# Kernel tuning notes

Measured on AMD Instinct MI355X. Metric: run time of the kernel, lower is better.

## Reference

```python
import jax, jax.numpy as jnp
import numpy as np

B, T, C, H = 8, 1024, 768, 12
HD = C // H  # head_dim = 64


def setup_inputs() -> dict:
    key = jax.random.key(0)
    ks = jax.random.split(key, 5)
    x = jax.random.normal(ks[0], (B, T, C), dtype=jnp.float32)
    mask = jnp.tril(jnp.ones((T, T), dtype=bool))[None, None, :, :]  # causal [1,1,T,T]
    # Dense params (flax Dense: y = x @ kernel + bias)
    W_qkv = jax.random.normal(ks[1], (C, 3 * C), dtype=jnp.float32) * (1.0 / np.sqrt(C))
    b_qkv = jnp.zeros((3 * C,), dtype=jnp.float32)
    W_proj = jax.random.normal(ks[2], (C, C), dtype=jnp.float32) * (1.0 / np.sqrt(C))
    b_proj = jnp.zeros((C,), dtype=jnp.float32)
    return {"x": x, "mask": mask, "W_qkv": W_qkv, "b_qkv": b_qkv,
            "W_proj": W_proj, "b_proj": b_proj}


def reference(x, mask, W_qkv, b_qkv, W_proj, b_proj):
    Bx, Tx, Cx = x.shape
    qkv = x @ W_qkv + b_qkv                      # [B, T, 3C]
    qkv = qkv.reshape(Bx, Tx, 3 * H, HD)
    q, k, v = jnp.array_split(qkv, 3, axis=2)    # each [B, T, H, HD]
    scale = 1.0 / jnp.sqrt(jnp.float32(HD))
    attn = jnp.einsum('bqhd,bkhd->bhqk', q, k) * scale  # [B, H, T, T]
    attn = jnp.where(mask, attn, jnp.finfo(jnp.float32).min)
    attn = jax.nn.softmax(attn, axis=-1)
    out = jnp.einsum('bhqk,bkhd->bqhd', attn, v).reshape(Bx, Tx, Cx)
    return out @ W_proj + b_proj
```

## Files before the change

kernel.cpp:

```cpp
#include <hip/hip_runtime.h>


typedef unsigned short u16;
typedef unsigned int u32;
typedef __bf16 bf16x8 __attribute__((ext_vector_type(8)));
typedef float  f32x4  __attribute__((ext_vector_type(4)));
typedef float  f32x16 __attribute__((ext_vector_type(16)));
typedef unsigned short u16x4 __attribute__((ext_vector_type(4)));
typedef unsigned short u16x8 __attribute__((ext_vector_type(8)));
typedef unsigned int u32x4 __attribute__((ext_vector_type(4)));

#define DEV static __device__ __forceinline__

constexpr int B_ = 8, T_ = 1024, C_ = 768, H_ = 12, HD_ = 64;
constexpr int M1 = B_ * T_;
constexpr int N1 = 3 * C_;
constexpr int KD = C_;

DEV u16 f2bf(float f) {
    union { float f; unsigned u; } v; v.f = f;
    unsigned r = v.u + 0x7fffu + ((v.u >> 16) & 1u);
    return (u16)(r >> 16);
}

DEV u16 bfbits(float f) {
    __bf16 h = (__bf16)f;
    union { __bf16 h; u16 u; } v; v.h = h;
    return v.u;
}

DEV u32 cvtpk(float lo, float hi) {
    u32 r;
    asm("v_cvt_pk_bf16_f32 %0, %1, %2" : "=v"(r) : "v"(lo), "v"(hi));
    return r;
}

DEV void gload16(const void* g, void* l) {
    __builtin_amdgcn_global_load_lds(
        (const __attribute__((address_space(1))) unsigned*)g,
        (__attribute__((address_space(3))) unsigned*)l, 16, 0, 0);
}

DEV float redmax16(f32x16 v) {
    float a0 = fmaxf(v[0], v[1]), a1 = fmaxf(v[2], v[3]);
    float a2 = fmaxf(v[4], v[5]), a3 = fmaxf(v[6], v[7]);
    float a4 = fmaxf(v[8], v[9]), a5 = fmaxf(v[10], v[11]);
    float a6 = fmaxf(v[12], v[13]), a7 = fmaxf(v[14], v[15]);
    float b0 = fmaxf(a0, a1), b1 = fmaxf(a2, a3);
    float b2 = fmaxf(a4, a5), b3 = fmaxf(a6, a7);
    return fmaxf(fmaxf(b0, b1), fmaxf(b2, b3));
}
DEV float redsum16(f32x16 v) {
    float a0 = v[0] + v[1], a1 = v[2] + v[3], a2 = v[4] + v[5], a3 = v[6] + v[7];
    float a4 = v[8] + v[9], a5 = v[10] + v[11], a6 = v[12] + v[13], a7 = v[14] + v[15];
    float b0 = a0 + a1, b1 = a2 + a3, b2 = a4 + a5, b3 = a6 + a7;
    return (b0 + b1) + (b2 + b3);
}


__global__ __launch_bounds__(256) void cvt_all_kern(
    const float* __restrict__ x, u16* __restrict__ xb,
    const float* __restrict__ Wq, const float* __restrict__ Wp,
    u16* __restrict__ WqT, u16* __restrict__ WpT) {
    __shared__ float tile[32][33];
    const int bid = blockIdx.x;
    if (bid < 3072) {
        const int i = bid * 256 + threadIdx.x;
        const float4* xf = (const float4*)x;
        float4 a = xf[i * 2], b = xf[i * 2 + 1];
        u16x8 o;
        o[0] = f2bf(a.x); o[1] = f2bf(a.y); o[2] = f2bf(a.z); o[3] = f2bf(a.w);
        o[4] = f2bf(b.x); o[5] = f2bf(b.y); o[6] = f2bf(b.z); o[7] = f2bf(b.w);
        *(u16x8*)(xb + (size_t)i * 8) = o;
        return;
    }
    const int wb = bid - 3072;
    int bx = wb % 96;
    const int k0 = (wb / 96) * 32;
    const float* W; u16* Wt; int N;
    if (bx < N1 / 32) { W = Wq; Wt = WqT; N = N1; }
    else { bx -= N1 / 32; W = Wp; Wt = WpT; N = C_; }
    const int n0 = bx * 32;
    const int tx = threadIdx.x & 31, ty = threadIdx.x >> 5;
#pragma unroll
    for (int i = 0; i < 4; i++) {
        int k = ty * 4 + i;
        tile[k][tx] = W[(size_t)(k0 + k) * N + n0 + tx];
    }
    __syncthreads();
#pragma unroll
    for (int i = 0; i < 4; i++) {
        int n = ty * 4 + i;
        Wt[(size_t)(n0 + n) * KD + k0 + tx] = f2bf(tile[tx][n]);
    }
}


template <int MODE>
__global__ __launch_bounds__(256, 2) void gemm_bt_kern(
    const u16* __restrict__ A, const u16* __restrict__ Bt,
    const float* __restrict__ bias, int nBN,
    u16* __restrict__ qw, u16* __restrict__ kw, u16* __restrict__ vw,
    float* __restrict__ out) {
    __shared__ u16 lds[16384];
    char* LA = (char*)lds;
    char* LB = (char*)lds + 16384;
    const int cpx = gridDim.x >> 3;
    const int bid = (blockIdx.x & 7) * cpx + (blockIdx.x >> 3);
    const int bm = bid / nBN, bn = bid % nBN;
    const int m0 = bm * 128, n0 = bn * 128;
    const int t = threadIdx.x;
    const int lane = t & 63, w = t >> 6;
    const int wr = w >> 1, wc = w & 1;
    const int l15 = lane & 15, lhi = lane >> 4;
    const int srow = t >> 3;
    const int scb = ((t & 7) << 4) ^ ((srow & 7) << 4);
    const char* Ab = (const char*)(A + (size_t)(m0 + srow) * KD) + scb;
    const char* Bb = (const char*)(Bt + (size_t)(n0 + srow) * KD) + scb;

    f32x4 acc[4][4] = {};

    for (int k0 = 0; k0 < KD; k0 += 64) {
#pragma unroll
        for (int s = 0; s < 4; s++) {
            gload16(Ab + (size_t)k0 * 2 + (size_t)s * 32 * KD * 2, LA + w * 1024 + s * 4096);
            gload16(Bb + (size_t)k0 * 2 + (size_t)s * 32 * KD * 2, LB + w * 1024 + s * 4096);
        }
        __syncthreads();
#pragma unroll
        for (int kk = 0; kk < 2; kk++) {
            bf16x8 af[4], bfr[4];
#pragma unroll
            for (int i = 0; i < 4; i++) {
                int rowA = wr * 64 + i * 16 + l15;
                af[i] = *(const bf16x8*)(LA + rowA * 128 +
                                         ((kk * 64 + lhi * 16) ^ ((rowA & 7) << 4)));
                int rowB = wc * 64 + i * 16 + l15;
                bfr[i] = *(const bf16x8*)(LB + rowB * 128 +
                                          ((kk * 64 + lhi * 16) ^ ((rowB & 7) << 4)));
            }
#pragma unroll
            for (int fm = 0; fm < 4; fm++)
#pragma unroll
                for (int fn = 0; fn < 4; fn++)
                    acc[fm][fn] = __builtin_amdgcn_mfma_f32_16x16x32_bf16(
                        af[fm], bfr[fn], acc[fm][fn], 0, 0, 0);
        }
        __syncthreads();
    }

    if constexpr (MODE == 1) {
#pragma unroll
        for (int fm = 0; fm < 4; fm++) {
            const int mb = m0 + wr * 64 + fm * 16 + lhi * 4;
#pragma unroll
            for (int fn = 0; fn < 4; fn++) {
                const int n = n0 + wc * 64 + fn * 16 + l15;
                const float bv = bias[n];
#pragma unroll
                for (int r = 0; r < 4; r++)
                    out[(size_t)(mb + r) * C_ + n] = acc[fm][fn][r] + bv;
            }
        }
    } else {
        char* TT = (char*)lds;
        const int typ = bn / 6;
        const int h0 = (bn % 6) * 2;
        if (typ < 2) {
            const float sc = (typ == 0) ? 0.125f * 1.44269504f : 1.0f;
#pragma unroll
            for (int fn = 0; fn < 4; fn++) {
                const int col = wc * 64 + fn * 16 + l15;
                const float bv = bias[n0 + col];
#pragma unroll
                for (int fm = 0; fm < 4; fm++) {
                    const int row0 = wr * 64 + fm * 16 + lhi * 4;
#pragma unroll
                    for (int r = 0; r < 4; r++) {
                        const int row = row0 + r;
                        *(u16*)(TT + row * 256 + ((col * 2) ^ ((row & 7) << 5))) =
                            bfbits((acc[fm][fn][r] + bv) * sc);
                    }
                }
            }
            __syncthreads();
            u16* dst = (typ == 0) ? qw : kw;
#pragma unroll
            for (int i = 0; i < 8; i++) {
                const int wk = t + 256 * i;
                const int m = wk >> 4, c = wk & 15;
                u16x8 v8 = *(u16x8*)(TT + m * 256 + ((c * 16) ^ ((m & 7) << 5)));
                const int mb = m0 + m, b = mb >> 10, tq = mb & 1023;
                const int h = h0 + (c >> 3), d0 = (c & 7) * 8;
                *(u16x8*)(dst + (((size_t)(b * H_ + h) * T_ + tq) << 6) + d0) = v8;
            }
        } else {
#pragma unroll
            for (int fn = 0; fn < 4; fn++) {
                const int col = wc * 64 + fn * 16 + l15;
                const float bv = bias[n0 + col];
                const int cx = (col & 7) << 4;
#pragma unroll
                for (int fm = 0; fm < 4; fm++) {
                    const int row0 = wr * 64 + fm * 16 + lhi * 4;
                    u16x4 pk;
#pragma unroll
                    for (int r = 0; r < 4; r++) pk[r] = bfbits(acc[fm][fn][r] + bv);
                    *(u16x4*)(TT + col * 256 + ((row0 * 2) ^ cx)) = pk;
                }
            }
            __syncthreads();
#pragma unroll
            for (int i = 0; i < 8; i++) {
                const int wk = t + 256 * i;
                const int col = wk >> 4, ch = wk & 15;
                u16x8 v8 = *(u16x8*)(TT + col * 256 + ((ch * 16) ^ ((col & 7) << 4)));
                const int b = m0 >> 10, tq0 = (m0 & 1023) + ch * 8;
                const int h = h0 + (col >> 6), d = col & 63;
                *(u16x8*)(vw + (((size_t)(b * H_ + h) * HD_ + d) << 10) + tq0) = v8;
            }
        }
    }
}


__global__ __launch_bounds__(256, 4) void attn_fwd_kern(
    const u16* __restrict__ qg, const u16* __restrict__ kg,
    const u16* __restrict__ vg, u16* __restrict__ ao) {
    __shared__ u16 kld[2][64 * 64];
    __shared__ u16 vld[2][64 * 64];
    const int n = blockIdx.x;
    const int bh = (n & 7) + 8 * ((n >> 3) % 12);
    const int qt = 7 - n / 96;
    const int t = threadIdx.x, lane = t & 63, w = t >> 6;
    const int q5 = lane & 31, h2 = lane >> 5;
    const int srow = t >> 3;
    const int scb = ((t & 7) << 4) ^ ((srow & 7) << 4);
    const char* kb = (const char*)(kg + (size_t)bh * T_ * HD_);
    const char* vb = (const char*)(vg + (size_t)bh * HD_ * T_);

    const int qrow_g = qt * 128 + w * 32 + q5;
    const u16* qrow = qg + (size_t)bh * T_ * HD_ + (size_t)qrow_g * HD_ + h2 * 8;
    bf16x8 qf[4];
#pragma unroll
    for (int kc = 0; kc < 4; kc++)
        qf[kc] = *(const bf16x8*)(qrow + kc * 16);

#pragma unroll
    for (int s = 0; s < 2; s++) {
        gload16(kb + (size_t)(srow + s * 32) * 128 + scb,
                (char*)kld[0] + w * 1024 + s * 4096);
        gload16(vb + (size_t)(srow + s * 32) * 2048 + scb,
                (char*)vld[0] + w * 1024 + s * 4096);
    }
    __syncthreads();

    f32x16 acc[2] = {};
    float mst = -1e30f, lst = 0.f;
    const int qmax = qt * 128 + w * 32 + 31;

    const int ntiles = 2 * qt + 2;
    for (int kvt = 0; kvt < ntiles; kvt++) {
        const int cur = kvt & 1;
        if (kvt + 1 < ntiles) {
#pragma unroll
            for (int s = 0; s < 2; s++) {
                gload16(kb + (size_t)((kvt + 1) * 64 + srow + s * 32) * 128 + scb,
                        (char*)kld[cur ^ 1] + w * 1024 + s * 4096);
                gload16(vb + (size_t)(srow + s * 32) * 2048 + (kvt + 1) * 128 + scb,
                        (char*)vld[cur ^ 1] + w * 1024 + s * 4096);
            }
        }
        if (kvt * 64 <= qmax) {
            const char* kbase = (const char*)kld[cur];
            const char* vbase = (const char*)vld[cur];
            f32x16 s0 = {}, s1 = {};
            __builtin_amdgcn_s_setprio(1);
#pragma unroll
            for (int kc = 0; kc < 4; kc++) {
                const int r0 = q5, r1 = 32 + q5;
                bf16x8 kf0 = *(const bf16x8*)(kbase + r0 * 128 +
                                              ((kc * 32 + h2 * 16) ^ ((r0 & 7) << 4)));
                bf16x8 kf1 = *(const bf16x8*)(kbase + r1 * 128 +
                                              ((kc * 32 + h2 * 16) ^ ((r1 & 7) << 4)));
                s0 = __builtin_amdgcn_mfma_f32_32x32x16_bf16(kf0, qf[kc], s0, 0, 0, 0);
                s1 = __builtin_amdgcn_mfma_f32_32x32x16_bf16(kf1, qf[kc], s1, 0, 0, 0);
            }
            __builtin_amdgcn_s_setprio(0);
            if (kvt * 64 + 63 > qt * 128 + w * 32) {
                const int qg_ = qrow_g, kvb0 = kvt * 64 + 4 * h2;
#pragma unroll
                for (int r = 0; r < 16; r++) {
                    const int kvo = (r & 3) + 8 * (r >> 2);
                    if (kvb0 + kvo > qg_) s0[r] = -1e30f;
                    if (kvb0 + 32 + kvo > qg_) s1[r] = -1e30f;
                }
            }
            float pmax = fmaxf(redmax16(s0), redmax16(s1));
            pmax = fmaxf(pmax, __shfl_xor(pmax, 32));
            if (!__all(pmax <= mst)) {
                const float mn = fmaxf(mst, pmax);
                const float corr = exp2f(mst - mn);
                mst = mn;
#pragma unroll
                for (int r = 0; r < 16; r++) { acc[0][r] *= corr; acc[1][r] *= corr; }
                lst *= corr;
            }
#pragma unroll
            for (int r = 0; r < 16; r++) {
                s0[r] = exp2f(s0[r] - mst);
                s1[r] = exp2f(s1[r] - mst);
            }
            float rs = redsum16(s0) + redsum16(s1);
            rs += __shfl_xor(rs, 32);
            lst += rs;
            u32 pw0[8], pw1[8];
#pragma unroll
            for (int i = 0; i < 4; i++) {
                pw0[i]     = cvtpk(s0[4 * i + 0], s0[4 * i + 1]);
                pw1[i]     = cvtpk(s0[4 * i + 2], s0[4 * i + 3]);
                pw0[i + 4] = cvtpk(s1[4 * i + 0], s1[4 * i + 1]);
                pw1[i + 4] = cvtpk(s1[4 * i + 2], s1[4 * i + 3]);
            }
            bf16x8 pf[4];
#pragma unroll
            for (int m = 0; m < 4; m++) {
                u32 a0 = pw0[2 * m], b0 = pw0[2 * m + 1];
                asm("v_permlane32_swap_b32 %0, %1" : "+v"(a0), "+v"(b0));
                u32 a1 = pw1[2 * m], b1 = pw1[2 * m + 1];
                asm("v_permlane32_swap_b32 %0, %1" : "+v"(a1), "+v"(b1));
                u32x4 wv; wv[0] = a0; wv[1] = a1; wv[2] = b0; wv[3] = b1;
                pf[m] = __builtin_bit_cast(bf16x8, wv);
            }
            __builtin_amdgcn_s_setprio(1);
#pragma unroll
            for (int m = 0; m < 4; m++) {
#pragma unroll
                for (int db = 0; db < 2; db++) {
                    const int rd = db * 32 + q5;
                    bf16x8 vf = *(const bf16x8*)(vbase + rd * 128 +
                                                 ((m * 32 + h2 * 16) ^ ((rd & 7) << 4)));
                    acc[db] = __builtin_amdgcn_mfma_f32_32x32x16_bf16(vf, pf[m], acc[db], 0, 0, 0);
                }
            }
            __builtin_amdgcn_s_setprio(0);
        }
        __syncthreads();
    }

    const int b = bh / H_, h = bh % H_;
    const float inv = 1.0f / lst;
    u16* orow = ao + (size_t)(b * T_ + qrow_g) * C_ + h * 64 + 4 * h2;
#pragma unroll
    for (int db = 0; db < 2; db++)
#pragma unroll
        for (int q2 = 0; q2 < 4; q2++) {
            u16x4 pk;
#pragma unroll
            for (int e = 0; e < 4; e++) pk[e] = bfbits(acc[db][q2 * 4 + e] * inv);
            *(u16x4*)(orow + db * 32 + q2 * 8) = pk;
        }
}


extern "C" void kernel_launch(void* const* d_in, const int* in_sizes, int n_in,
                              void* d_out, int out_size, void* d_ws, size_t ws_size,
                              hipStream_t stream) {
    const float* x     = (const float*)d_in[0];
    const float* Wqkv  = (const float*)d_in[2];
    const float* bqkv  = (const float*)d_in[3];
    const float* Wproj = (const float*)d_in[4];
    const float* bproj = (const float*)d_in[5];
    float* out = (float*)d_out;

    char* ws = (char*)d_ws;
    u16* xb     = (u16*)(ws);
    u16* wqkvT  = (u16*)(ws + 12582912);
    u16* wprojT = (u16*)(ws + 16121856);
    u16* qw     = (u16*)(ws + 17301504);
    u16* kw     = (u16*)(ws + 29884416);
    u16* vw     = (u16*)(ws + 42467328);
    u16* ao     = (u16*)(ws + 55050240);

    cvt_all_kern<<<5376, 256, 0, stream>>>(x, xb, Wqkv, Wproj, wqkvT, wprojT);

    gemm_bt_kern<0><<<(M1 / 128) * (N1 / 128), 256, 0, stream>>>(
        xb, wqkvT, bqkv, N1 / 128, qw, kw, vw, nullptr);

    attn_fwd_kern<<<B_ * H_ * (T_ / 128), 256, 0, stream>>>(qw, kw, vw, ao);

    gemm_bt_kern<1><<<(M1 / 128) * (C_ / 128), 256, 0, stream>>>(
        ao, wprojT, bproj, C_ / 128, nullptr, nullptr, nullptr, out);
}
```

Measured before the change: 102.9 us.

## Split attention KV range in two per query tile and merge partials

Each causal query tile's KV loop is split into two halves run by separate blocks, doubling the grid to improve load balance and occupancy across CUs. Each half writes a normalized bf16 partial output plus its running max and sum, and a new merge kernel combines them with softmax rescaling into the head-interleaved layout. This costs extra global traffic for partials, an extra kernel launch, and an additional bf16 rounding of partial outputs. The split path is enabled only when the workspace is large enough, and it reuses the xb buffer for one partial.

```diff
diff --git a/kernel.cpp b/kernel.cpp
--- a/kernel.cpp
+++ b/kernel.cpp
@@ -16,6 +16,7 @@
 constexpr int M1 = B_ * T_;
 constexpr int N1 = 3 * C_;
 constexpr int KD = C_;
+constexpr int NROW = B_ * H_ * T_;
 
 DEV u16 f2bf(float f) {
     union { float f; unsigned u; } v; v.f = f;
@@ -27,6 +28,11 @@
     __bf16 h = (__bf16)f;
     union { __bf16 h; u16 u; } v; v.h = h;
     return v.u;
+}
+
+DEV float bf2f(u16 x) {
+    union { u32 u; float f; } v; v.u = (u32)x << 16;
+    return v.f;
 }
 
 DEV u32 cvtpk(float lo, float hi) {
@@ -224,14 +230,26 @@
 }
 
 
+template <int SPLIT>
 __global__ __launch_bounds__(256, 4) void attn_fwd_kern(
     const u16* __restrict__ qg, const u16* __restrict__ kg,
-    const u16* __restrict__ vg, u16* __restrict__ ao) {
+    const u16* __restrict__ vg, u16* __restrict__ ao,
+    u16* __restrict__ On0, u16* __restrict__ On1, float* __restrict__ ml) {
     __shared__ u16 kld[2][64 * 64];
     __shared__ u16 vld[2][64 * 64];
     const int n = blockIdx.x;
     const int bh = (n & 7) + 8 * ((n >> 3) % 12);
-    const int qt = 7 - n / 96;
+    int qt, sp, k0t, k1t;
+    if constexpr (SPLIT) {
+        const int rem = n / 96;
+        qt = 7 - (rem >> 1);
+        sp = rem & 1;
+        k0t = sp ? (qt + 1) : 0;
+        k1t = sp ? (2 * qt + 2) : (qt + 1);
+    } else {
+        qt = 7 - n / 96;
+        sp = 0; k0t = 0; k1t = 2 * qt + 2;
+    }
     const int t = threadIdx.x, lane = t & 63, w = t >> 6;
     const int q5 = lane & 31, h2 = lane >> 5;
     const int srow = t >> 3;
@@ -248,9 +266,9 @@
 
 #pragma unroll
     for (int s = 0; s < 2; s++) {
-        gload16(kb + (size_t)(srow + s * 32) * 128 + scb,
+        gload16(kb + (size_t)(k0t * 64 + srow + s * 32) * 128 + scb,
                 (char*)kld[0] + w * 1024 + s * 4096);
-        gload16(vb + (size_t)(srow + s * 32) * 2048 + scb,
+        gload16(vb + (size_t)(srow + s * 32) * 2048 + k0t * 128 + scb,
                 (char*)vld[0] + w * 1024 + s * 4096);
     }
     __syncthreads();
@@ -259,10 +277,9 @@
     float mst = -1e30f, lst = 0.f;
     const int qmax = qt * 128 + w * 32 + 31;
 
-    const int ntiles = 2 * qt + 2;
-    for (int kvt = 0; kvt < ntiles; kvt++) {
-        const int cur = kvt & 1;
-        if (kvt + 1 < ntiles) {
+    for (int kvt = k0t; kvt < k1t; kvt++) {
+        const int cur = (kvt - k0t) & 1;
+        if (kvt + 1 < k1t) {
 #pragma unroll
             for (int s = 0; s < 2; s++) {
                 gload16(kb + (size_t)((kvt + 1) * 64 + srow + s * 32) * 128 + scb,
@@ -288,12 +305,12 @@
             }
             __builtin_amdgcn_s_setprio(0);
             if (kvt * 64 + 63 > qt * 128 + w * 32) {
-                const int qg_ = qrow_g, kvb0 = kvt * 64 + 4 * h2;
+                const int kvb0 = kvt * 64 + 4 * h2;
 #pragma unroll
                 for (int r = 0; r < 16; r++) {
                     const int kvo = (r & 3) + 8 * (r >> 2);
-                    if (kvb0 + kvo > qg_) s0[r] = -1e30f;
-                    if (kvb0 + 32 + kvo > qg_) s1[r] = -1e30f;
+                    if (kvb0 + kvo > qrow_g) s0[r] = -1e30f;
+                    if (kvb0 + 32 + kvo > qrow_g) s1[r] = -1e30f;
                 }
             }
             float pmax = fmaxf(redmax16(s0), redmax16(s1));
@@ -348,18 +365,61 @@
         __syncthreads();
     }
 
+    if constexpr (SPLIT) {
+        const float inv = (lst > 0.f) ? 1.0f / lst : 0.f;
+        u16* Onp = sp ? On1 : On0;
+        u16* orow = Onp + (((size_t)(bh * T_ + qrow_g)) << 6) + 4 * h2;
+#pragma unroll
+        for (int db = 0; db < 2; db++)
+#pragma unroll
+            for (int q2 = 0; q2 < 4; q2++) {
+                u16x4 pk;
+#pragma unroll
+                for (int e = 0; e < 4; e++) pk[e] = bfbits(acc[db][q2 * 4 + e] * inv);
+                *(u16x4*)(orow + db * 32 + q2 * 8) = pk;
+            }
+        if (h2 == 0) {
+            const size_t row = (size_t)bh * T_ + qrow_g;
+            ml[(size_t)(sp * 2 + 0) * NROW + row] = mst;
+            ml[(size_t)(sp * 2 + 1) * NROW + row] = lst;
+        }
+    } else {
+        const int b = bh / H_, h = bh % H_;
+        const float inv = 1.0f / lst;
+        u16* orow = ao + (size_t)(b * T_ + qrow_g) * C_ + h * 64 + 4 * h2;
+#pragma unroll
+        for (int db = 0; db < 2; db++)
+#pragma unroll
+            for (int q2 = 0; q2 < 4; q2++) {
+                u16x4 pk;
+#pragma unroll
+                for (int e = 0; e < 4; e++) pk[e] = bfbits(acc[db][q2 * 4 + e] * inv);
+                *(u16x4*)(orow + db * 32 + q2 * 8) = pk;
+            }
+    }
+}
+
+
+__global__ __launch_bounds__(256) void attn_merge_kern(
+    const u16* __restrict__ On0, const u16* __restrict__ On1,
+    const float* __restrict__ ml, u16* __restrict__ ao) {
+    const int idx = blockIdx.x * 256 + threadIdx.x;
+    const int row = idx >> 3, c = idx & 7;
+    const int bh = row >> 10, tq = row & 1023;
     const int b = bh / H_, h = bh % H_;
-    const float inv = 1.0f / lst;
-    u16* orow = ao + (size_t)(b * T_ + qrow_g) * C_ + h * 64 + 4 * h2;
-#pragma unroll
-    for (int db = 0; db < 2; db++)
-#pragma unroll
-        for (int q2 = 0; q2 < 4; q2++) {
-            u16x4 pk;
-#pragma unroll
-            for (int e = 0; e < 4; e++) pk[e] = bfbits(acc[db][q2 * 4 + e] * inv);
-            *(u16x4*)(orow + db * 32 + q2 * 8) = pk;
-        }
+    const float m0 = ml[row],            l0 = ml[NROW + row];
+    const float m1 = ml[2 * NROW + row], l1 = ml[3 * NROW + row];
+    const float mf = fmaxf(m0, m1);
+    float w0 = l0 * exp2f(m0 - mf), w1 = l1 * exp2f(m1 - mf);
+    const float inv = 1.0f / (w0 + w1);
+    w0 *= inv; w1 *= inv;
+    u16x8 a0 = *(const u16x8*)(On0 + ((size_t)row << 6) + c * 8);
+    u16x8 a1 = *(const u16x8*)(On1 + ((size_t)row << 6) + c * 8);
+    u16x8 o;
+#pragma unroll
+    for (int e = 0; e < 8; e++)
+        o[e] = bfbits(w0 * bf2f(a0[e]) + w1 * bf2f(a1[e]));
+    *(u16x8*)(ao + (size_t)(b * T_ + tq) * C_ + h * 64 + c * 8) = o;
 }
 
 
@@ -381,13 +441,24 @@
     u16* kw     = (u16*)(ws + 29884416);
     u16* vw     = (u16*)(ws + 42467328);
     u16* ao     = (u16*)(ws + 55050240);
+    u16* On0    = (u16*)(ws + 67633152);
+    float* ml   = (float*)(ws + 80216064);
+    const bool split = ws_size >= 81788928ULL;
 
     cvt_all_kern<<<5376, 256, 0, stream>>>(x, xb, Wqkv, Wproj, wqkvT, wprojT);
 
     gemm_bt_kern<0><<<(M1 / 128) * (N1 / 128), 256, 0, stream>>>(
         xb, wqkvT, bqkv, N1 / 128, qw, kw, vw, nullptr);
 
-    attn_fwd_kern<<<B_ * H_ * (T_ / 128), 256, 0, stream>>>(qw, kw, vw, ao);
+    if (split) {
+        u16* On1 = xb;
+        attn_fwd_kern<1><<<B_ * H_ * (T_ / 128) * 2, 256, 0, stream>>>(
+            qw, kw, vw, nullptr, On0, On1, ml);
+        attn_merge_kern<<<(NROW * 8) / 256, 256, 0, stream>>>(On0, On1, ml, ao);
+    } else {
+        attn_fwd_kern<0><<<B_ * H_ * (T_ / 128), 256, 0, stream>>>(
+            qw, kw, vw, ao, nullptr, nullptr, nullptr);
+    }
 
     gemm_bt_kern<1><<<(M1 / 128) * (C_ / 128), 256, 0, stream>>>(
         ao, wprojT, bproj, C_ / 128, nullptr, nullptr, nullptr, out);
```

After: 107.7 us. 1.05x slower.
